# Kernel optimization log

Measured on AMD Instinct MI355X. Metric: run time of the kernel, lower is better.

The kernel has to match this reference:

```python
import jax, jax.numpy as jnp
import numpy as np

B, S, H, KV, D, HID = 1, 2048, 32, 8, 128, 4096
SCALE = D ** -0.5
EPS = 1e-5
QMAX = 127.0  # 8-bit symmetric fake quant


def fake_quant(x):
    # per-tensor symmetric int8 fake quantization with straight-through estimator
    s = jnp.maximum(jnp.max(jnp.abs(x)), 1e-5) / QMAX
    q = jnp.clip(jnp.round(x / s), -QMAX - 1.0, QMAX) * s
    return x + jax.lax.stop_gradient(q - x)


def rms_norm(x, w):
    xf = x.astype(jnp.float32)
    var = jnp.mean(xf * xf, axis=-1, keepdims=True)
    return (xf * jax.lax.rsqrt(var + EPS)).astype(x.dtype) * w


def rotate_half(x):
    h = x.shape[-1] // 2
    return jnp.concatenate([-x[..., h:], x[..., :h]], axis=-1)


def qlinear(x, W):
    # QuantLinear: fake-quant activation and weight, then matmul (no bias)
    return fake_quant(x) @ fake_quant(W).T


def setup_inputs() -> dict:
    key = jax.random.key(0)
    ks = jax.random.split(key, 5)
    hidden_states = jax.random.normal(ks[0], (B, S, HID), jnp.float32)
    # RoPE tables
    inv_freq = 1.0 / (10000.0 ** (np.arange(0, D, 2, dtype=np.float32) / D))
    freqs = np.outer(np.arange(S, dtype=np.float32), inv_freq)  # [S, D/2]
    emb = np.concatenate([freqs, freqs], axis=-1)  # [S, D]
    cos = jnp.asarray(np.cos(emb))[None]  # [1,S,D]
    sin = jnp.asarray(np.sin(emb))[None]
    # causal additive mask [1,1,S,S]
    mask = jnp.where(np.tril(np.ones((S, S), dtype=bool)), 0.0, -1e9).astype(jnp.float32)[None, None]
    Wq = jax.random.normal(ks[1], (H * D, HID), jnp.float32) * 0.02
    Wk = jax.random.normal(ks[2], (KV * D, HID), jnp.float32) * 0.02
    Wv = jax.random.normal(ks[3], (KV * D, HID), jnp.float32) * 0.02
    Wo = jax.random.normal(ks[4], (HID, H * D), jnp.float32) * 0.02
    q_norm_w = jnp.ones((D,), jnp.float32)
    k_norm_w = jnp.ones((D,), jnp.float32)
    return dict(hidden_states=hidden_states, cos=cos, sin=sin, attention_mask=mask,
                Wq=Wq, Wk=Wk, Wv=Wv, Wo=Wo, q_norm_w=q_norm_w, k_norm_w=k_norm_w)


def reference(hidden_states, cos, sin, attention_mask, Wq, Wk, Wv, Wo, q_norm_w, k_norm_w):
    b, s, _ = hidden_states.shape
    q = qlinear(hidden_states, Wq).reshape(b, s, H, D).transpose(0, 2, 1, 3)   # [B,H,S,D]
    k = qlinear(hidden_states, Wk).reshape(b, s, KV, D).transpose(0, 2, 1, 3)  # [B,KV,S,D]
    v = qlinear(hidden_states, Wv).reshape(b, s, KV, D).transpose(0, 2, 1, 3)
    q = rms_norm(q, q_norm_w)
    k = rms_norm(k, k_norm_w)
    c = cos[:, None]  # unsqueeze head dim -> [1,1,S,D]
    sn = sin[:, None]
    q = q * c + rotate_half(q) * sn
    k = k * c + rotate_half(k) * sn
    n_rep = H // KV
    k = jnp.repeat(k, n_rep, axis=1)  # [B,H,S,D]
    v = jnp.repeat(v, n_rep, axis=1)
    # fake-quant around QK^T
    q = fake_quant(q)
    k = fake_quant(k)
    scores = jnp.einsum('bhqd,bhkd->bhqk', q, k) * SCALE + attention_mask
    p = jax.nn.softmax(scores.astype(jnp.float32), axis=-1).astype(q.dtype)
    # fake-quant around PV
    p = fake_quant(p)
    v = fake_quant(v)
    out = jnp.einsum('bhqk,bhkd->bhqd', p, v)
    out = out.transpose(0, 2, 1, 3).reshape(b, s, H * D)
    return qlinear(out, Wo)
```

## Files before the change

kernel.cpp:

```cpp
#include <hip/hip_runtime.h>
#include <hip/hip_bf16.h>
#include <math.h>
#include <stdint.h>

#define S_LEN 2048
#define NH    32
#define NKV   8
#define HD    128
#define HIDD  4096

typedef unsigned short u16;
typedef __attribute__((ext_vector_type(4))) int i32x4;

#define GLD16(g, l) __builtin_amdgcn_global_load_lds( \
    (const __attribute__((address_space(1))) void*)(g), \
    (__attribute__((address_space(3))) void*)(l), 16, 0, 0)


__device__ __forceinline__ float slot_scale(const unsigned* slot) {
    return fmaxf(__uint_as_float(*slot), 1e-5f) / 127.0f;
}

__device__ __forceinline__ float exp2_fast(float x) {
    float r; asm("v_exp_f32 %0, %1" : "=v"(r) : "v"(x)); return r;
}
__device__ __forceinline__ float log2_fast(float x) {
    float r; asm("v_log_f32 %0, %1" : "=v"(r) : "v"(x)); return r;
}

__device__ __forceinline__ int qint(float x, float s) {
    float q = rintf(x / s);
    q = fminf(fmaxf(q, -128.0f), 127.0f);
    return (int)q;
}

__device__ __forceinline__ void block_amax_atomic(float m, unsigned* slot) {
    __shared__ float wmax[8];
    const int lane = threadIdx.x & 63;
    const int wid  = threadIdx.x >> 6;
    const int nw   = blockDim.x >> 6;
    #pragma unroll
    for (int o = 32; o; o >>= 1) m = fmaxf(m, __shfl_xor(m, o));
    if (lane == 0) wmax[wid] = m;
    __syncthreads();
    if (threadIdx.x == 0) {
        float bm = wmax[0];
        for (int i = 1; i < nw; ++i) bm = fmaxf(bm, wmax[i]);
        atomicMax(slot, __float_as_uint(bm));
    }
}

struct Amax5Args { const float* p[5]; size_t n4[5]; };
__global__ __launch_bounds__(256) void absmax5_kernel(Amax5Args a, unsigned* slots) {
    const int t = blockIdx.y;
    const float4* x4 = (const float4*)a.p[t];
    const size_t n4 = a.n4[t];
    size_t i = (size_t)blockIdx.x * blockDim.x + threadIdx.x;
    size_t stride = (size_t)gridDim.x * blockDim.x;
    float m = 0.0f;
    for (; i < n4; i += stride) {
        float4 v = x4[i];
        m = fmaxf(m, fmaxf(fmaxf(fabsf(v.x), fabsf(v.y)), fmaxf(fabsf(v.z), fabsf(v.w))));
    }
    block_amax_atomic(m, slots + t);
}

struct Quant5Args { const float* p[5]; char* o[5]; size_t n4[5]; };
__global__ __launch_bounds__(256) void quant5_kernel(Quant5Args a, const unsigned* slots) {
    const int t = blockIdx.y;
    float s = slot_scale(slots + t);
    const float4* x4 = (const float4*)a.p[t];
    unsigned* o4 = (unsigned*)a.o[t];
    const size_t n4 = a.n4[t];
    size_t i = (size_t)blockIdx.x * blockDim.x + threadIdx.x;
    size_t stride = (size_t)gridDim.x * blockDim.x;
    for (; i < n4; i += stride) {
        float4 v = x4[i];
        unsigned o = (unsigned)(qint(v.x, s) & 255)
                   | ((unsigned)(qint(v.y, s) & 255) << 8)
                   | ((unsigned)(qint(v.z, s) & 255) << 16)
                   | ((unsigned)(qint(v.w, s) & 255) << 24);
        o4[i] = o;
    }
}

__global__ __launch_bounds__(256) void quant_kernel(const float* __restrict__ x,
                                                    size_t n4, const unsigned* slot,
                                                    char* __restrict__ out) {
    float s = slot_scale(slot);
    size_t i = (size_t)blockIdx.x * blockDim.x + threadIdx.x;
    size_t stride = (size_t)gridDim.x * blockDim.x;
    const float4* x4 = (const float4*)x;
    unsigned* o4 = (unsigned*)out;
    for (; i < n4; i += stride) {
        float4 v = x4[i];
        unsigned o = (unsigned)(qint(v.x, s) & 255)
                   | ((unsigned)(qint(v.y, s) & 255) << 8)
                   | ((unsigned)(qint(v.z, s) & 255) << 16)
                   | ((unsigned)(qint(v.w, s) & 255) << 24);
        o4[i] = o;
    }
}

__device__ __forceinline__ void gemm_body(const char* __restrict__ A,
                                          const char* __restrict__ B,
                                          float* __restrict__ C,
                                          int m0, int n0, int N, int K,
                                          float scale, unsigned* out_amax,
                                          char* Asm, char* Bsm) {
    const int tid  = threadIdx.x;
    const int lane = tid & 63;
    const int wave = tid >> 6;
    const int wr = (wave >> 1) * 64;
    const int wc = (wave & 1) * 64;
    const int l15 = lane & 15;
    const int l4  = lane >> 4;
    const int cx  = (l4 ^ (l15 & 3)) * 16;
    const int r0  = tid >> 2;
    const int sc  = ((tid & 3) ^ ((tid >> 2) & 3)) * 16;

    i32x4 acc[4][4];
    #pragma unroll
    for (int i = 0; i < 4; ++i)
        #pragma unroll
        for (int j = 0; j < 4; ++j) acc[i][j] = (i32x4){0, 0, 0, 0};

    auto STAGE = [&](int buf, int k0) {
        GLD16(&A[(size_t)(m0 + r0) * K + k0 + sc],      &Asm[buf * 8192 + wave * 1024]);
        GLD16(&A[(size_t)(m0 + 64 + r0) * K + k0 + sc], &Asm[buf * 8192 + 4096 + wave * 1024]);
        GLD16(&B[(size_t)(n0 + r0) * K + k0 + sc],      &Bsm[buf * 8192 + wave * 1024]);
        GLD16(&B[(size_t)(n0 + 64 + r0) * K + k0 + sc], &Bsm[buf * 8192 + 4096 + wave * 1024]);
    };

    const int NT = K >> 6;
    STAGE(0, 0);
    STAGE(1, 64);
    int cur = 0;
    for (int t = 0; t < NT; ++t) {
        if (t + 1 < NT) {
            asm volatile("s_waitcnt vmcnt(4)" ::: "memory");
        } else {
            asm volatile("s_waitcnt vmcnt(0)" ::: "memory");
        }
        __builtin_amdgcn_sched_barrier(0);
        __builtin_amdgcn_s_barrier();
        __builtin_amdgcn_sched_barrier(0);
        if (t + 2 < NT) {
            int nb = cur + 2; if (nb >= 3) nb -= 3;
            STAGE(nb, (t + 2) << 6);
        }
        i32x4 af[4], bfr[4];
        #pragma unroll
        for (int i = 0; i < 4; ++i)
            af[i] = *(const i32x4*)&Asm[cur * 8192 + (wr + i * 16 + l15) * 64 + cx];
        #pragma unroll
        for (int j = 0; j < 4; ++j)
            bfr[j] = *(const i32x4*)&Bsm[cur * 8192 + (wc + j * 16 + l15) * 64 + cx];
        #pragma unroll
        for (int i = 0; i < 4; ++i)
            #pragma unroll
            for (int j = 0; j < 4; ++j)
                acc[i][j] = __builtin_amdgcn_mfma_i32_16x16x64_i8(af[i], bfr[j], acc[i][j], 0, 0, 0);
        cur += 1; if (cur == 3) cur = 0;
    }

    float lm = 0.0f;
    #pragma unroll
    for (int i = 0; i < 4; ++i)
        #pragma unroll
        for (int j = 0; j < 4; ++j)
            #pragma unroll
            for (int r = 0; r < 4; ++r) {
                int row = m0 + wr + i * 16 + l4 * 4 + r;
                int col = n0 + wc + j * 16 + l15;
                float v = (float)acc[i][j][r] * scale;
                C[(size_t)row * N + col] = v;
                lm = fmaxf(lm, fabsf(v));
            }
    __syncthreads();
    if (out_amax) block_amax_atomic(lm, out_amax);
}

__global__ __launch_bounds__(256) void gemm_qkv_kernel(const char* __restrict__ Aq,
                                                       const char* __restrict__ Wqq,
                                                       const char* __restrict__ Wkq,
                                                       const char* __restrict__ Wvq,
                                                       float* __restrict__ qf,
                                                       float* __restrict__ kf,
                                                       float* __restrict__ vf,
                                                       const unsigned* __restrict__ slots,
                                                       unsigned* v_amax) {
    __shared__ __align__(16) char Asm[3 * 8192];
    __shared__ __align__(16) char Bsm[3 * 8192];
    int bid = blockIdx.x;
    int swz = (bid & 7) * 96 + (bid >> 3);
    int x = swz & 15, y = swz >> 4;
    const char* B; float* C; int N, nb; const unsigned* sB; unsigned* am = nullptr;
    if (y < 32)      { B = Wqq; C = qf; N = NH * HD;  nb = y;      sB = slots + 1; }
    else if (y < 40) { B = Wkq; C = kf; N = NKV * HD; nb = y - 32; sB = slots + 2; }
    else             { B = Wvq; C = vf; N = NKV * HD; nb = y - 40; sB = slots + 3; am = v_amax; }
    float scale = slot_scale(slots + 0) * slot_scale(sB);
    gemm_body(Aq, B, C, x * 128, nb * 128, N, HIDD, scale, am, Asm, Bsm);
}

__global__ __launch_bounds__(256) void gemm_o_kernel(const char* __restrict__ A,
                                                     const char* __restrict__ Woq,
                                                     float* __restrict__ C,
                                                     const unsigned* __restrict__ slots) {
    __shared__ __align__(16) char Asm[3 * 8192];
    __shared__ __align__(16) char Bsm[3 * 8192];
    int bid = blockIdx.x;
    int swz = (bid & 7) * 64 + (bid >> 3);
    int x = swz & 15, y = swz >> 4;
    float scale = slot_scale(slots + 8) * slot_scale(slots + 4);
    gemm_body(A, Woq, C, x * 128, y * 128, NH * HD, HIDD, scale, nullptr, Asm, Bsm);
}

__global__ __launch_bounds__(256) void rmsrope2_kernel(float* __restrict__ qx,
                                                       float* __restrict__ kx,
                                                       const float* __restrict__ cosb,
                                                       const float* __restrict__ sinb,
                                                       const float* __restrict__ qw,
                                                       const float* __restrict__ kw,
                                                       unsigned* slots) {
    const int which = blockIdx.y;
    float* x = which ? kx : qx;
    const float* w = which ? kw : qw;
    const int s_shift = which ? 3 : 5;
    const int nrows = which ? (S_LEN * NKV) : (S_LEN * NH);
    unsigned* slot = slots + (which ? 6 : 5);

    const int lane = threadIdx.x & 63;
    const int wid  = threadIdx.x >> 6;
    const float wa = w[lane];
    const float wb = w[lane + 64];
    float lm = 0.0f;
    for (int row = blockIdx.x * 4 + wid; row < nrows; row += gridDim.x * 4) {
        int s = row >> s_shift;
        float* xr = x + (size_t)row * 128;
        float a = xr[lane], b = xr[lane + 64];
        float ss = a * a + b * b;
        #pragma unroll
        for (int o = 32; o; o >>= 1) ss += __shfl_xor(ss, o);
        float inv = 1.0f / sqrtf(ss * (1.0f / 128.0f) + 1e-5f);
        float ya = (a * inv) * wa;
        float yb = (b * inv) * wb;
        const float* cr = cosb + (size_t)s * 128;
        const float* sr = sinb + (size_t)s * 128;
        float o0 = ya * cr[lane]      - yb * sr[lane];
        float o1 = yb * cr[lane + 64] + ya * sr[lane + 64];
        xr[lane] = o0;
        xr[lane + 64] = o1;
        lm = fmaxf(lm, fmaxf(fabsf(o0), fabsf(o1)));
    }
    block_amax_atomic(lm, slot);
}

__global__ __launch_bounds__(256) void quant_qk2_kernel(const float* __restrict__ qx,
                                                        const float* __restrict__ kx,
                                                        const unsigned* slots,
                                                        char* __restrict__ qq,
                                                        char* __restrict__ kq) {
    int tid = blockIdx.x * 256 + threadIdx.x;
    const int qtot4 = S_LEN * NH * HD / 4;
    if (tid < qtot4) {
        float s = slot_scale(slots + 5);
        int e = tid * 4;
        int d  = e & 127;
        int h  = (e >> 7) & 31;
        int sp = e >> 12;
        float4 v = *(const float4*)&qx[e];
        uchar4 o;
        o.x = (unsigned char)qint(v.x, s); o.y = (unsigned char)qint(v.y, s);
        o.z = (unsigned char)qint(v.z, s); o.w = (unsigned char)qint(v.w, s);
        *(uchar4*)&qq[((size_t)h * S_LEN + sp) * 128 + d] = o;
    } else {
        tid -= qtot4;
        float s = slot_scale(slots + 6);
        int e = tid * 4;
        int d  = e & 127;
        int h  = (e >> 7) & 7;
        int sp = e >> 10;
        float4 v = *(const float4*)&kx[e];
        uchar4 o;
        o.x = (unsigned char)qint(v.x, s); o.y = (unsigned char)qint(v.y, s);
        o.z = (unsigned char)qint(v.z, s); o.w = (unsigned char)qint(v.w, s);
        *(uchar4*)&kq[((size_t)h * S_LEN + sp) * 128 + d] = o;
    }
}

__global__ __launch_bounds__(256) void quant_v_kernel(const float* __restrict__ x,
                                                      const unsigned* slot,
                                                      char* __restrict__ out) {
    __shared__ unsigned char t8[64][36];
    const float s = slot_scale(slot);
    const int t   = threadIdx.x;
    const int sp0 = blockIdx.x * 64;
    const int d0  = blockIdx.y * 32;
    const int kvh = blockIdx.z;
    const int dl = t & 31;
    const int sb = t >> 5;
    #pragma unroll
    for (int j = 0; j < 8; ++j) {
        int spl = sb + j * 8;
        float v = x[((size_t)(sp0 + spl) * NKV + kvh) * 128 + d0 + dl];
        t8[spl][dl] = (unsigned char)qint(v, s);
    }
    __syncthreads();
    const int dd = t >> 3;
    const int ch = t & 7;
    unsigned lo = 0, hi = 0;
    #pragma unroll
    for (int j = 0; j < 4; ++j) lo |= (unsigned)t8[ch * 8 + j][dd] << (8 * j);
    #pragma unroll
    for (int j = 0; j < 4; ++j) hi |= (unsigned)t8[ch * 8 + 4 + j][dd] << (8 * j);
    *(uint2*)&out[((size_t)kvh * 128 + d0 + dd) * S_LEN + sp0 + ch * 8] = make_uint2(lo, hi);
}

__global__ __launch_bounds__(512) void attn_kernel(const char* __restrict__ Qq,
                                                   const char* __restrict__ Kq,
                                                   const char* __restrict__ Vt,
                                                   const unsigned* sq_slot,
                                                   const unsigned* sk_slot,
                                                   const unsigned* sv_slot,
                                                   float* __restrict__ O,
                                                   unsigned* amax_slot) {
    __shared__ __align__(16) char Klds[64 * 144];
    __shared__ __align__(16) char Vlds[128 * 80];
    __shared__ __align__(16) char plds[8][16 * 80];

    const int tid  = threadIdx.x;
    const int lane = tid & 63;
    const int wave = tid >> 6;
    const int mw   = wave & 3;
    const int h  = blockIdx.y;
    const int kv = h >> 2;
    const int l15 = lane & 15;
    const int l4  = lane >> 4;
    const size_t kvS = (size_t)kv * S_LEN;

    const int qtS = blockIdx.x;
    const int qtB = 31 - qtS;
    const int my_qt = (wave < 4) ? qtB : qtS;
    const int qr0 = my_qt * 64 + mw * 16;

    const float sq = slot_scale(sq_slot);
    const float sk = slot_scale(sk_slot);
    const float sv = slot_scale(sv_slot);
    const float qs2 = sq * sk * 0.08838834764831845f * 1.4426950408889634f;
    const float osc = (1.0f / 127.0f) * sv;
    const float NEG = -1e30f;

    const int krow = tid >> 3, kcol = (tid & 7) * 16;
    const int vrow = tid >> 2, vcol = (tid & 3) * 16;

    i32x4 qf2[2];
    {
        const char* qp = Qq + ((size_t)h * S_LEN + qr0 + l15) * 128 + l4 * 16;
        qf2[0] = *(const i32x4*)(qp);
        qf2[1] = *(const i32x4*)(qp + 64);
    }

    auto qk_block = [&](int hb) -> i32x4 {
        i32x4 sacc = {0, 0, 0, 0};
        #pragma unroll
        for (int c = 0; c < 2; ++c) {
            i32x4 kfa = *(const i32x4*)&Klds[(hb * 16 + l15) * 144 + c * 64 + l4 * 16];
            sacc = __builtin_amdgcn_mfma_i32_16x16x64_i8(kfa, qf2[c], sacc, 0, 0, 0);
        }
        return sacc;
    };

    float m_l = NEG, l_l = 0.0f;

    auto p1_interior = [&](int hb) {
        i32x4 sacc = qk_block(hb);
        float x0 = (float)sacc[0] * qs2, x1 = (float)sacc[1] * qs2;
        float x2 = (float)sacc[2] * qs2, x3 = (float)sacc[3] * qs2;
        float bm = fmaxf(fmaxf(x0, x1), fmaxf(x2, x3));
        float mn = fmaxf(m_l, bm);
        float ps = exp2_fast(x0 - mn) + exp2_fast(x1 - mn)
                 + exp2_fast(x2 - mn) + exp2_fast(x3 - mn);
        l_l = l_l * exp2_fast(m_l - mn) + ps;
        m_l = mn;
    };
    auto p1_diag = [&](int hb) {
        i32x4 sacc = qk_block(hb);
        float x[4];
        #pragma unroll
        for (int r = 0; r < 4; ++r) {
            float v = (float)sacc[r] * qs2;
            x[r] = ((l4 * 4 + r) > l15) ? NEG : v;
        }
        float bm = fmaxf(fmaxf(x[0], x[1]), fmaxf(x[2], x[3]));
        float mn = fmaxf(m_l, bm);
        float ps = exp2_fast(x[0] - mn) + exp2_fast(x[1] - mn)
                 + exp2_fast(x[2] - mn) + exp2_fast(x[3] - mn);
        l_l = l_l * exp2_fast(m_l - mn) + ps;
        m_l = mn;
    };

    i32x4 kreg = *(const i32x4*)&Kq[(kvS + krow) * 128 + kcol];
    #pragma unroll 1
    for (int kc = 0; kc <= qtB; ++kc) {
        __syncthreads();
        *(i32x4*)&Klds[krow * 144 + kcol] = kreg;
        __syncthreads();
        if (kc < qtB)
            kreg = *(const i32x4*)&Kq[(kvS + (kc + 1) * 64 + krow) * 128 + kcol];
        if (kc < my_qt) {
            p1_interior(0); p1_interior(1); p1_interior(2); p1_interior(3);
        } else if (kc == my_qt) {
            #pragma unroll
            for (int hb = 0; hb < 4; ++hb) {
                if (hb < mw) p1_interior(hb);
                else if (hb == mw) p1_diag(hb);
            }
        }
    }
    float cmy;
    {
        float m2 = fmaxf(m_l, __shfl_xor(m_l, 16));
        float mfin = fmaxf(m2, __shfl_xor(m2, 32));
        float t = l_l * exp2_fast(m_l - mfin);
        t += __shfl_xor(t, 16);
        t += __shfl_xor(t, 32);
        cmy = mfin - log2_fast(127.0f / t);
    }

    i32x4 oacc[8];
    #pragma unroll
    for (int dt = 0; dt < 8; ++dt) oacc[dt] = (i32x4){0, 0, 0, 0};

    auto p2_interior = [&](int hb) -> unsigned {
        i32x4 sacc = qk_block(hb);
        unsigned pack = 0;
        #pragma unroll
        for (int r = 0; r < 4; ++r) {
            float pq = rintf(exp2_fast(fmaf((float)sacc[r], qs2, -cmy)));
            pack |= ((unsigned)(int)pq) << (8 * r);
        }
        return pack;
    };
    auto p2_diag = [&](int hb) -> unsigned {
        i32x4 sacc = qk_block(hb);
        unsigned pack = 0;
        #pragma unroll
        for (int r = 0; r < 4; ++r) {
            float p = exp2_fast(fmaf((float)sacc[r], qs2, -cmy));
            float pq = ((l4 * 4 + r) > l15) ? 0.0f : rintf(p);
            pack |= ((unsigned)(int)pq) << (8 * r);
        }
        return pack;
    };
    auto pv8 = [&]() {
        i32x4 pf = *(const i32x4*)&plds[wave][l15 * 80 + l4 * 16];
        __builtin_amdgcn_s_setprio(1);
        #pragma unroll
        for (int dt = 0; dt < 8; ++dt) {
            i32x4 vfb = *(const i32x4*)&Vlds[(dt * 16 + l15) * 80 + l4 * 16];
            oacc[dt] = __builtin_amdgcn_mfma_i32_16x16x64_i8(pf, vfb, oacc[dt], 0, 0, 0);
        }
        __builtin_amdgcn_s_setprio(0);
    };

    kreg = *(const i32x4*)&Kq[(kvS + krow) * 128 + kcol];
    i32x4 vreg = *(const i32x4*)&Vt[((size_t)kv * 128 + vrow) * S_LEN + vcol];
    #pragma unroll 1
    for (int kc = 0; kc <= qtB; ++kc) {
        __syncthreads();
        *(i32x4*)&Klds[krow * 144 + kcol] = kreg;
        *(i32x4*)&Vlds[vrow * 80 + vcol] = vreg;
        __syncthreads();
        if (kc < qtB) {
            kreg = *(const i32x4*)&Kq[(kvS + (kc + 1) * 64 + krow) * 128 + kcol];
            vreg = *(const i32x4*)&Vt[((size_t)kv * 128 + vrow) * S_LEN + (kc + 1) * 64 + vcol];
        }
        if (kc < my_qt) {
            #pragma unroll
            for (int hb = 0; hb < 4; ++hb)
                *(unsigned*)&plds[wave][l15 * 80 + hb * 16 + l4 * 4] = p2_interior(hb);
            pv8();
        } else if (kc == my_qt) {
            #pragma unroll
            for (int hb = 0; hb < 4; ++hb) {
                unsigned pack = 0;
                if (hb < mw) pack = p2_interior(hb);
                else if (hb == mw) pack = p2_diag(hb);
                *(unsigned*)&plds[wave][l15 * 80 + hb * 16 + l4 * 4] = pack;
            }
            pv8();
        }
    }

    float lm = 0.0f;
    #pragma unroll
    for (int dt = 0; dt < 8; ++dt)
        #pragma unroll
        for (int r = 0; r < 4; ++r) {
            float v = (float)oacc[dt][r] * osc;
            O[(size_t)(qr0 + l4 * 4 + r) * (NH * 128) + h * 128 + dt * 16 + l15] = v;
            lm = fmaxf(lm, fabsf(v));
        }
    block_amax_atomic(lm, amax_slot);
}

extern "C" void kernel_launch(void* const* d_in, const int* in_sizes, int n_in,
                              void* d_out, int out_size, void* d_ws, size_t ws_size,
                              hipStream_t stream) {
    const float* hs   = (const float*)d_in[0];
    const float* cosb = (const float*)d_in[1];
    const float* sinb = (const float*)d_in[2];
    const float* Wq   = (const float*)d_in[4];
    const float* Wk   = (const float*)d_in[5];
    const float* Wv   = (const float*)d_in[6];
    const float* Wo   = (const float*)d_in[7];
    const float* qnw  = (const float*)d_in[8];
    const float* knw  = (const float*)d_in[9];
    float* out = (float*)d_out;

    char* ws = (char*)d_ws;
    unsigned* slots = (unsigned*)ws;
    size_t off = 256;
    auto take = [&](size_t bytes) { size_t o = off; off += (bytes + 255) & ~(size_t)255; return o; };
    char*  hsq  = (char*)(ws + take((size_t)S_LEN * HIDD));
    char*  Wqq  = (char*)(ws + take((size_t)NH * HD * HIDD));
    char*  Wkq  = (char*)(ws + take((size_t)NKV * HD * HIDD));
    char*  Wvq  = (char*)(ws + take((size_t)NKV * HD * HIDD));
    char*  Woq  = (char*)(ws + take((size_t)HIDD * NH * HD));
    float* qf   = (float*)(ws + take((size_t)S_LEN * NH * HD * 4));
    float* kf   = (float*)(ws + take((size_t)S_LEN * NKV * HD * 4));
    float* vf   = (float*)(ws + take((size_t)S_LEN * NKV * HD * 4));
    char*  qq   = (char*)(ws + take((size_t)NH * S_LEN * HD));
    char*  kq   = (char*)(ws + take((size_t)NKV * S_LEN * HD));
    char*  vtq  = (char*)(ws + take((size_t)NKV * HD * S_LEN));
    float* attnf = qf;
    char*  attnq = hsq;

    hipMemsetAsync(ws, 0, 64, stream);

    const size_t n_hs = (size_t)S_LEN * HIDD;
    const size_t n_wq = (size_t)NH * HD * HIDD;
    const size_t n_wk = (size_t)NKV * HD * HIDD;

    Amax5Args aa;
    aa.p[0] = hs; aa.p[1] = Wq; aa.p[2] = Wk; aa.p[3] = Wv; aa.p[4] = Wo;
    aa.n4[0] = n_hs / 4; aa.n4[1] = n_wq / 4; aa.n4[2] = n_wk / 4;
    aa.n4[3] = n_wk / 4; aa.n4[4] = n_wq / 4;
    absmax5_kernel<<<dim3(512, 5), 256, 0, stream>>>(aa, slots);

    Quant5Args qa;
    qa.p[0] = hs; qa.p[1] = Wq; qa.p[2] = Wk; qa.p[3] = Wv; qa.p[4] = Wo;
    qa.o[0] = hsq; qa.o[1] = Wqq; qa.o[2] = Wkq; qa.o[3] = Wvq; qa.o[4] = Woq;
    qa.n4[0] = n_hs / 4; qa.n4[1] = n_wq / 4; qa.n4[2] = n_wk / 4;
    qa.n4[3] = n_wk / 4; qa.n4[4] = n_wq / 4;
    quant5_kernel<<<dim3(1024, 5), 256, 0, stream>>>(qa, slots);

    gemm_qkv_kernel<<<768, 256, 0, stream>>>(hsq, Wqq, Wkq, Wvq, qf, kf, vf,
                                             slots, slots + 7);

    rmsrope2_kernel<<<dim3(1024, 2), 256, 0, stream>>>(qf, kf, cosb, sinb, qnw, knw, slots);

    quant_qk2_kernel<<<10240, 256, 0, stream>>>(qf, kf, slots, qq, kq);
    quant_v_kernel<<<dim3(32, 4, 8), 256, 0, stream>>>(vf, slots + 7, vtq);

    attn_kernel<<<dim3(16, NH), 512, 0, stream>>>(qq, kq, vtq,
                                                  slots + 5, slots + 6, slots + 7,
                                                  attnf, slots + 8);

    quant_kernel<<<2048, 256, 0, stream>>>(attnf, n_hs / 4, slots + 8, attnq);
    gemm_o_kernel<<<512, 256, 0, stream>>>(attnq, Woq, out, slots);
    (void)in_sizes; (void)n_in; (void)out_size; (void)ws_size;
}
```

Before: 343.3 us.

## Fuse RMSNorm+RoPE into QKV GEMM epilogue and merge Q/K/V quant kernels

The QKV GEMM's warp tiling changes so each wave owns 32 full rows across all 128 columns of a head. That lets the epilogue compute the per-head RMS norm through lane shuffles, apply RoPE, and record the amax, which removes the separate rmsrope2 pass that read and wrote q/k in fp32. The V transpose-quant kernel and the Q/K quant kernel are merged into one launch. In exchange each wave now holds 2x8 accumulator tiles and reads all eight B fragments, which changes register pressure and LDS read patterns.

```diff
diff --git a/kernel.cpp b/kernel.cpp
--- a/kernel.cpp
+++ b/kernel.cpp
@@ -106,7 +106,7 @@
                                           const char* __restrict__ B,
                                           float* __restrict__ C,
                                           int m0, int n0, int N, int K,
-                                          float scale, unsigned* out_amax,
+                                          float scale,
                                           char* Asm, char* Bsm) {
     const int tid  = threadIdx.x;
     const int lane = tid & 63;
@@ -164,7 +164,6 @@
         cur += 1; if (cur == 3) cur = 0;
     }
 
-    float lm = 0.0f;
     #pragma unroll
     for (int i = 0; i < 4; ++i)
         #pragma unroll
@@ -173,12 +172,8 @@
             for (int r = 0; r < 4; ++r) {
                 int row = m0 + wr + i * 16 + l4 * 4 + r;
                 int col = n0 + wc + j * 16 + l15;
-                float v = (float)acc[i][j][r] * scale;
-                C[(size_t)row * N + col] = v;
-                lm = fmaxf(lm, fabsf(v));
+                C[(size_t)row * N + col] = (float)acc[i][j][r] * scale;
             }
-    __syncthreads();
-    if (out_amax) block_amax_atomic(lm, out_amax);
 }
 
 __global__ __launch_bounds__(256) void gemm_qkv_kernel(const char* __restrict__ Aq,
@@ -188,19 +183,132 @@
                                                        float* __restrict__ qf,
                                                        float* __restrict__ kf,
                                                        float* __restrict__ vf,
-                                                       const unsigned* __restrict__ slots,
-                                                       unsigned* v_amax) {
+                                                       const float* __restrict__ cosb,
+                                                       const float* __restrict__ sinb,
+                                                       const float* __restrict__ qnw,
+                                                       const float* __restrict__ knw,
+                                                       unsigned* __restrict__ slots) {
     __shared__ __align__(16) char Asm[3 * 8192];
     __shared__ __align__(16) char Bsm[3 * 8192];
+    const int tid  = threadIdx.x;
+    const int lane = tid & 63;
+    const int wave = tid >> 6;
+    const int l15 = lane & 15;
+    const int l4  = lane >> 4;
+    const int cx  = (l4 ^ (l15 & 3)) * 16;
+    const int r0  = tid >> 2;
+    const int sc  = ((tid & 3) ^ ((tid >> 2) & 3)) * 16;
+    const int wr  = wave * 32;
+
     int bid = blockIdx.x;
     int swz = (bid & 7) * 96 + (bid >> 3);
     int x = swz & 15, y = swz >> 4;
-    const char* B; float* C; int N, nb; const unsigned* sB; unsigned* am = nullptr;
-    if (y < 32)      { B = Wqq; C = qf; N = NH * HD;  nb = y;      sB = slots + 1; }
-    else if (y < 40) { B = Wkq; C = kf; N = NKV * HD; nb = y - 32; sB = slots + 2; }
-    else             { B = Wvq; C = vf; N = NKV * HD; nb = y - 40; sB = slots + 3; am = v_amax; }
-    float scale = slot_scale(slots + 0) * slot_scale(sB);
-    gemm_body(Aq, B, C, x * 128, nb * 128, N, HIDD, scale, am, Asm, Bsm);
+    const char* B; float* C; int N, nb, kind; const unsigned* sB; const float* w;
+    if (y < 32)      { B = Wqq; C = qf; N = NH * HD;  nb = y;      sB = slots + 1; kind = 0; w = qnw; }
+    else if (y < 40) { B = Wkq; C = kf; N = NKV * HD; nb = y - 32; sB = slots + 2; kind = 1; w = knw; }
+    else             { B = Wvq; C = vf; N = NKV * HD; nb = y - 40; sB = slots + 3; kind = 2; w = nullptr; }
+    const float scale = slot_scale(slots + 0) * slot_scale(sB);
+    const int m0 = x * 128, n0 = nb * 128;
+
+    i32x4 acc[2][8];
+    #pragma unroll
+    for (int i = 0; i < 2; ++i)
+        #pragma unroll
+        for (int j = 0; j < 8; ++j) acc[i][j] = (i32x4){0, 0, 0, 0};
+
+    auto STAGE = [&](int buf, int k0) {
+        GLD16(&Aq[(size_t)(m0 + r0) * HIDD + k0 + sc],     &Asm[buf * 8192 + wave * 1024]);
+        GLD16(&Aq[(size_t)(m0 + 64 + r0) * HIDD + k0 + sc],&Asm[buf * 8192 + 4096 + wave * 1024]);
+        GLD16(&B[(size_t)(n0 + r0) * HIDD + k0 + sc],      &Bsm[buf * 8192 + wave * 1024]);
+        GLD16(&B[(size_t)(n0 + 64 + r0) * HIDD + k0 + sc], &Bsm[buf * 8192 + 4096 + wave * 1024]);
+    };
+
+    const int NT = HIDD >> 6;
+    STAGE(0, 0);
+    STAGE(1, 64);
+    int cur = 0;
+    for (int t = 0; t < NT; ++t) {
+        if (t + 1 < NT) {
+            asm volatile("s_waitcnt vmcnt(4)" ::: "memory");
+        } else {
+            asm volatile("s_waitcnt vmcnt(0)" ::: "memory");
+        }
+        __builtin_amdgcn_sched_barrier(0);
+        __builtin_amdgcn_s_barrier();
+        __builtin_amdgcn_sched_barrier(0);
+        if (t + 2 < NT) {
+            int nb3 = cur + 2; if (nb3 >= 3) nb3 -= 3;
+            STAGE(nb3, (t + 2) << 6);
+        }
+        i32x4 af[2], bfr[8];
+        #pragma unroll
+        for (int i = 0; i < 2; ++i)
+            af[i] = *(const i32x4*)&Asm[cur * 8192 + (wr + i * 16 + l15) * 64 + cx];
+        #pragma unroll
+        for (int j = 0; j < 8; ++j)
+            bfr[j] = *(const i32x4*)&Bsm[cur * 8192 + (j * 16 + l15) * 64 + cx];
+        #pragma unroll
+        for (int i = 0; i < 2; ++i)
+            #pragma unroll
+            for (int j = 0; j < 8; ++j)
+                acc[i][j] = __builtin_amdgcn_mfma_i32_16x16x64_i8(af[i], bfr[j], acc[i][j], 0, 0, 0);
+        cur += 1; if (cur == 3) cur = 0;
+    }
+
+    float lm = 0.0f;
+    if (kind == 2) {
+        #pragma unroll
+        for (int i = 0; i < 2; ++i)
+            #pragma unroll
+            for (int r = 0; r < 4; ++r) {
+                int row = m0 + wr + i * 16 + l4 * 4 + r;
+                #pragma unroll
+                for (int j = 0; j < 8; ++j) {
+                    float v = (float)acc[i][j][r] * scale;
+                    C[(size_t)row * N + n0 + j * 16 + l15] = v;
+                    lm = fmaxf(lm, fabsf(v));
+                }
+            }
+        __syncthreads();
+        block_amax_atomic(lm, slots + 7);
+    } else {
+        float wj[8];
+        #pragma unroll
+        for (int j = 0; j < 8; ++j) wj[j] = w[j * 16 + l15];
+        #pragma unroll
+        for (int i = 0; i < 2; ++i)
+            #pragma unroll
+            for (int r = 0; r < 4; ++r) {
+                int row = m0 + wr + i * 16 + l4 * 4 + r;
+                float v[8];
+                float ss = 0.0f;
+                #pragma unroll
+                for (int j = 0; j < 8; ++j) {
+                    v[j] = (float)acc[i][j][r] * scale;
+                    ss += v[j] * v[j];
+                }
+                ss += __shfl_xor(ss, 1);
+                ss += __shfl_xor(ss, 2);
+                ss += __shfl_xor(ss, 4);
+                ss += __shfl_xor(ss, 8);
+                float inv = 1.0f / sqrtf(ss * (1.0f / 128.0f) + 1e-5f);
+                const float* cr = cosb + (size_t)row * 128;
+                const float* sr = sinb + (size_t)row * 128;
+                float yv[8];
+                #pragma unroll
+                for (int j = 0; j < 8; ++j) yv[j] = v[j] * inv * wj[j];
+                #pragma unroll
+                for (int j = 0; j < 8; ++j) {
+                    int col = j * 16 + l15;
+                    float o = (j < 4) ? yv[j] * cr[col] - yv[j + 4] * sr[col]
+                                      : yv[j] * cr[col] + yv[j - 4] * sr[col];
+                    C[(size_t)row * N + n0 + col] = o;
+                    lm = fmaxf(lm, fabsf(o));
+                }
+            }
+        __syncthreads();
+        block_amax_atomic(lm, slots + (kind == 0 ? 5 : 6));
+    }
 }
 
 __global__ __launch_bounds__(256) void gemm_o_kernel(const char* __restrict__ A,
@@ -213,55 +321,45 @@
     int swz = (bid & 7) * 64 + (bid >> 3);
     int x = swz & 15, y = swz >> 4;
     float scale = slot_scale(slots + 8) * slot_scale(slots + 4);
-    gemm_body(A, Woq, C, x * 128, y * 128, NH * HD, HIDD, scale, nullptr, Asm, Bsm);
-}
-
-__global__ __launch_bounds__(256) void rmsrope2_kernel(float* __restrict__ qx,
-                                                       float* __restrict__ kx,
-                                                       const float* __restrict__ cosb,
-                                                       const float* __restrict__ sinb,
-                                                       const float* __restrict__ qw,
-                                                       const float* __restrict__ kw,
-                                                       unsigned* slots) {
-    const int which = blockIdx.y;
-    float* x = which ? kx : qx;
-    const float* w = which ? kw : qw;
-    const int s_shift = which ? 3 : 5;
-    const int nrows = which ? (S_LEN * NKV) : (S_LEN * NH);
-    unsigned* slot = slots + (which ? 6 : 5);
-
-    const int lane = threadIdx.x & 63;
-    const int wid  = threadIdx.x >> 6;
-    const float wa = w[lane];
-    const float wb = w[lane + 64];
-    float lm = 0.0f;
-    for (int row = blockIdx.x * 4 + wid; row < nrows; row += gridDim.x * 4) {
-        int s = row >> s_shift;
-        float* xr = x + (size_t)row * 128;
-        float a = xr[lane], b = xr[lane + 64];
-        float ss = a * a + b * b;
-        #pragma unroll
-        for (int o = 32; o; o >>= 1) ss += __shfl_xor(ss, o);
-        float inv = 1.0f / sqrtf(ss * (1.0f / 128.0f) + 1e-5f);
-        float ya = (a * inv) * wa;
-        float yb = (b * inv) * wb;
-        const float* cr = cosb + (size_t)s * 128;
-        const float* sr = sinb + (size_t)s * 128;
-        float o0 = ya * cr[lane]      - yb * sr[lane];
-        float o1 = yb * cr[lane + 64] + ya * sr[lane + 64];
-        xr[lane] = o0;
-        xr[lane + 64] = o1;
-        lm = fmaxf(lm, fmaxf(fabsf(o0), fabsf(o1)));
-    }
-    block_amax_atomic(lm, slot);
-}
-
-__global__ __launch_bounds__(256) void quant_qk2_kernel(const float* __restrict__ qx,
+    gemm_body(A, Woq, C, x * 128, y * 128, NH * HD, HIDD, scale, Asm, Bsm);
+}
+
+__global__ __launch_bounds__(256) void quant_qkv_kernel(const float* __restrict__ qx,
                                                         const float* __restrict__ kx,
+                                                        const float* __restrict__ vx,
                                                         const unsigned* slots,
                                                         char* __restrict__ qq,
-                                                        char* __restrict__ kq) {
-    int tid = blockIdx.x * 256 + threadIdx.x;
+                                                        char* __restrict__ kq,
+                                                        char* __restrict__ vtq) {
+    const int bx = blockIdx.x;
+    if (bx < 1024) {
+        __shared__ unsigned char t8[64][36];
+        const float s = slot_scale(slots + 7);
+        const int t   = threadIdx.x;
+        const int kvh = bx >> 7;
+        const int rem = bx & 127;
+        const int d0  = (rem & 3) * 32;
+        const int sp0 = (rem >> 2) * 64;
+        const int dl = t & 31;
+        const int sb = t >> 5;
+        #pragma unroll
+        for (int j = 0; j < 8; ++j) {
+            int spl = sb + j * 8;
+            float v = vx[((size_t)(sp0 + spl) * NKV + kvh) * 128 + d0 + dl];
+            t8[spl][dl] = (unsigned char)qint(v, s);
+        }
+        __syncthreads();
+        const int dd = t >> 3;
+        const int ch = t & 7;
+        unsigned lo = 0, hi = 0;
+        #pragma unroll
+        for (int j = 0; j < 4; ++j) lo |= (unsigned)t8[ch * 8 + j][dd] << (8 * j);
+        #pragma unroll
+        for (int j = 0; j < 4; ++j) hi |= (unsigned)t8[ch * 8 + 4 + j][dd] << (8 * j);
+        *(uint2*)&vtq[((size_t)kvh * 128 + d0 + dd) * S_LEN + sp0 + ch * 8] = make_uint2(lo, hi);
+        return;
+    }
+    int tid = (bx - 1024) * 256 + threadIdx.x;
     const int qtot4 = S_LEN * NH * HD / 4;
     if (tid < qtot4) {
         float s = slot_scale(slots + 5);
@@ -289,34 +387,6 @@
     }
 }
 
-__global__ __launch_bounds__(256) void quant_v_kernel(const float* __restrict__ x,
-                                                      const unsigned* slot,
-                                                      char* __restrict__ out) {
-    __shared__ unsigned char t8[64][36];
-    const float s = slot_scale(slot);
-    const int t   = threadIdx.x;
-    const int sp0 = blockIdx.x * 64;
-    const int d0  = blockIdx.y * 32;
-    const int kvh = blockIdx.z;
-    const int dl = t & 31;
-    const int sb = t >> 5;
-    #pragma unroll
-    for (int j = 0; j < 8; ++j) {
-        int spl = sb + j * 8;
-        float v = x[((size_t)(sp0 + spl) * NKV + kvh) * 128 + d0 + dl];
-        t8[spl][dl] = (unsigned char)qint(v, s);
-    }
-    __syncthreads();
-    const int dd = t >> 3;
-    const int ch = t & 7;
-    unsigned lo = 0, hi = 0;
-    #pragma unroll
-    for (int j = 0; j < 4; ++j) lo |= (unsigned)t8[ch * 8 + j][dd] << (8 * j);
-    #pragma unroll
-    for (int j = 0; j < 4; ++j) hi |= (unsigned)t8[ch * 8 + 4 + j][dd] << (8 * j);
-    *(uint2*)&out[((size_t)kvh * 128 + d0 + dd) * S_LEN + sp0 + ch * 8] = make_uint2(lo, hi);
-}
-
 __global__ __launch_bounds__(512) void attn_kernel(const char* __restrict__ Qq,
                                                    const char* __restrict__ Kq,
                                                    const char* __restrict__ Vt,
@@ -557,12 +627,9 @@
     quant5_kernel<<<dim3(1024, 5), 256, 0, stream>>>(qa, slots);
 
     gemm_qkv_kernel<<<768, 256, 0, stream>>>(hsq, Wqq, Wkq, Wvq, qf, kf, vf,
-                                             slots, slots + 7);
-
-    rmsrope2_kernel<<<dim3(1024, 2), 256, 0, stream>>>(qf, kf, cosb, sinb, qnw, knw, slots);
-
-    quant_qk2_kernel<<<10240, 256, 0, stream>>>(qf, kf, slots, qq, kq);
-    quant_v_kernel<<<dim3(32, 4, 8), 256, 0, stream>>>(vf, slots + 7, vtq);
+                                             cosb, sinb, qnw, knw, slots);
+
+    quant_qkv_kernel<<<1024 + 10240, 256, 0, stream>>>(qf, kf, vf, slots, qq, kq, vtq);
 
     attn_kernel<<<dim3(16, NH), 512, 0, stream>>>(qq, kq, vtq,
                                                   slots + 5, slots + 6, slots + 7,
```

Result: no change. 343.5 us (+0.1%).
